# Performance work log

Measured on AMD Instinct MI355X. Metric: run time of the kernel, lower is better.

The kernel has to match this reference:

```python
import jax, jax.numpy as jnp
import numpy as np

B, S, D, H = 2, 2048, 1024, 16
HD = D // H  # head dim = 64


def setup_inputs() -> dict:
    key = jax.random.key(0)
    k1, k2, k3, k4 = jax.random.split(key, 4)
    x = jax.random.normal(k1, (B, S, D), dtype=jnp.float32)
    context = jax.random.normal(k2, (B, S, D), dtype=jnp.float32)
    Wq = jax.random.normal(k3, (D, D), dtype=jnp.float32) * 0.02   # to_query weight [out,in]
    Wkv = jax.random.normal(k4, (2 * D, D), dtype=jnp.float32) * 0.02  # to_key_value weight [out,in]
    return {"x": x, "context": context, "Wq": Wq, "Wkv": Wkv}


def reference(x, context, Wq, Wkv):
    b, i, _ = x.shape
    j = context.shape[1]
    # projections (torch Linear: y = x @ W.T)
    q = x @ Wq.T                      # [b, i, D]
    kv = context @ Wkv.T              # [b, j, 2D]
    k, v = kv[..., :D], kv[..., D:]
    # split heads: (h c) ordering -> reshape last dim to [H, HD]
    q = q.reshape(b, i, H, HD).transpose(0, 2, 1, 3)  # [b,h,i,c]
    k = k.reshape(b, j, H, HD).transpose(0, 2, 1, 3)  # [b,h,j,c]
    v = v.reshape(b, j, H, HD).transpose(0, 2, 1, 3)  # [b,h,j,c]
    q = q * (HD ** -0.5)
    scores = jnp.einsum('bhic,bhjc->bhij', q, k)      # [b,h,i,j]
    scores = scores - jax.lax.stop_gradient(scores.max(axis=-1, keepdims=True))
    attn = jax.nn.softmax(scores, axis=-1)
    out = jnp.einsum('bhij,bhjc->bhic', attn, v)      # [b,h,i,c]
    out = out.transpose(0, 2, 1, 3).reshape(b, i, H * HD)  # 'b h n d -> b n (h d)'
    return out
```

## Files before the change

### kernel.cpp

```cpp
#include <hip/hip_runtime.h>
#include <hip/hip_bf16.h>
#include <stdint.h>

typedef unsigned short u16;
typedef __attribute__((ext_vector_type(8))) __bf16 bf16x8;
typedef __attribute__((ext_vector_type(4))) float f32x4;
typedef __attribute__((ext_vector_type(16))) float f32x16;

#define AS1(p) ((const __attribute__((address_space(1))) void*)(p))
#define AS3(p) ((__attribute__((address_space(3))) void*)(p))

__device__ __forceinline__ u16 f2bf(float f) {
  union { float f; uint32_t u; } c; c.f = f;
  uint32_t u = c.u;
  u += 0x7fffu + ((u >> 16) & 1u);
  return (u16)(u >> 16);
}

__device__ __forceinline__ float exp2_fast(float x) {
  float r; asm("v_exp_f32 %0, %1" : "=v"(r) : "v"(x)); return r;
}

__global__ __launch_bounds__(256) void cast4_f32_bf16(
    const float4* __restrict__ s0, ushort4* __restrict__ d0, int n0,
    const float4* __restrict__ s1, ushort4* __restrict__ d1, int n1,
    const float4* __restrict__ s2, ushort4* __restrict__ d2, int n2,
    const float4* __restrict__ s3, ushort4* __restrict__ d3, int n3) {
  int bid = blockIdx.x;
  const float4* src; ushort4* dst; int n4, b0, nb;
  if (bid < 512)       { src = s0; dst = d0; n4 = n0; b0 = 0;    nb = 512; }
  else if (bid < 1024) { src = s1; dst = d1; n4 = n1; b0 = 512;  nb = 512; }
  else if (bid < 1152) { src = s2; dst = d2; n4 = n2; b0 = 1024; nb = 128; }
  else                 { src = s3; dst = d3; n4 = n3; b0 = 1152; nb = 256; }
  int stride = nb * 256;
  for (int i = (bid - b0) * 256 + threadIdx.x; i < n4; i += stride) {
    float4 v = src[i];
    ushort4 o;
    o.x = f2bf(v.x); o.y = f2bf(v.y); o.z = f2bf(v.z); o.w = f2bf(v.w);
    dst[i] = o;
  }
}

__global__ __launch_bounds__(256) void gemm_fused(const u16* __restrict__ xb,
                                                  const u16* __restrict__ wqb,
                                                  u16* __restrict__ qo,
                                                  const u16* __restrict__ cb,
                                                  const u16* __restrict__ wkb,
                                                  u16* __restrict__ kvo,
                                                  float scale_q) {
  __shared__ u16 As[3][128 * 32];
  __shared__ u16 Bs[3][128 * 32];
  const int K = 1024;
  int bid = (blockIdx.x & 7) * 96 + (blockIdx.x >> 3);
  const u16 *A, *B; u16* C; int N, bm, bn; float scale;
  if (bid < 256) { A = xb; B = wqb; C = qo;  N = 1024; bm = bid >> 3; bn = bid & 7;  scale = scale_q; }
  else { int b2 = bid - 256; A = cb; B = wkb; C = kvo; N = 2048; bm = b2 >> 4; bn = b2 & 15; scale = 1.0f; }

  int tid = threadIdx.x;
  int w = tid >> 6, l = tid & 63;
  int wr = w >> 1, wc = w & 1;
  int lr = l & 15, lg = l >> 4;

  const u16* Abase = A + (size_t)(bm * 128 + (l >> 2)) * K + (l & 3) * 8;
  const u16* Bbase = B + (size_t)(bn * 128 + (l >> 2)) * K + (l & 3) * 8;

  f32x4 acc[4][4];
#pragma unroll
  for (int i = 0; i < 4; ++i)
#pragma unroll
    for (int j = 0; j < 4; ++j) acc[i][j] = (f32x4){0.f, 0.f, 0.f, 0.f};

#define STAGE(buf, k0)                                                              \
  {                                                                                 \
    _Pragma("unroll")                                                               \
    for (int t2 = 0; t2 < 2; ++t2) {                                                \
      int seg = w * 2 + t2;                                                         \
      __builtin_amdgcn_global_load_lds(AS1(Abase + (size_t)seg * 16 * K + (k0)),    \
                                       AS3(&As[buf][seg * 512]), 16, 0, 0);         \
      __builtin_amdgcn_global_load_lds(AS1(Bbase + (size_t)seg * 16 * K + (k0)),    \
                                       AS3(&Bs[buf][seg * 512]), 16, 0, 0);         \
    }                                                                               \
  }

  STAGE(0, 0);
  STAGE(1, 32);
  int cur = 0;
  for (int t = 0; t < 32; ++t) {
    if (t < 30) {
      int pf = cur + 2; if (pf >= 3) pf -= 3;
      STAGE(pf, (t + 2) * 32);
      asm volatile("s_waitcnt vmcnt(8)" ::: "memory");
    } else if (t == 30) {
      asm volatile("s_waitcnt vmcnt(4)" ::: "memory");
    } else {
      asm volatile("s_waitcnt vmcnt(0)" ::: "memory");
    }
    __builtin_amdgcn_s_barrier();
    bf16x8 af[4], bb[4];
#pragma unroll
    for (int i = 0; i < 4; ++i)
      af[i] = *(const bf16x8*)(&As[cur][(wr * 64 + i * 16 + lr) * 32 + lg * 8]);
#pragma unroll
    for (int j = 0; j < 4; ++j)
      bb[j] = *(const bf16x8*)(&Bs[cur][(wc * 64 + j * 16 + lr) * 32 + lg * 8]);
    asm volatile("s_waitcnt lgkmcnt(0)" ::: "memory");
    __builtin_amdgcn_sched_barrier(0);
#pragma unroll
    for (int i = 0; i < 4; ++i)
#pragma unroll
      for (int j = 0; j < 4; ++j)
        acc[i][j] = __builtin_amdgcn_mfma_f32_16x16x32_bf16(af[i], bb[j], acc[i][j], 0, 0, 0);
    __builtin_amdgcn_s_barrier();
    if (++cur == 3) cur = 0;
  }
#undef STAGE

#pragma unroll
  for (int i = 0; i < 4; ++i)
#pragma unroll
    for (int j = 0; j < 4; ++j)
#pragma unroll
      for (int r = 0; r < 4; ++r) {
        int row = bm * 128 + wr * 64 + i * 16 + lg * 4 + r;
        int col = bn * 128 + wc * 64 + j * 16 + lr;
        C[(size_t)row * N + col] = f2bf(acc[i][j][r] * scale);
      }
}

#define SQ 2048
#define NTT 16

__global__ __launch_bounds__(256, 2) void attn_kernel(const u16* __restrict__ Q,
                                                      const u16* __restrict__ KV,
                                                      float* __restrict__ O) {
  __shared__ u16 Ks[2][128 * 64];
  __shared__ u16 Vt[64 * 128];

  int wgid = (blockIdx.x & 7) * 64 + (blockIdx.x >> 3);
  int qt = wgid & 15;
  int bh = wgid >> 4;
  int b = bh >> 4, h = bh & 15;
  int tid = threadIdx.x;
  int w = tid >> 6, l = tid & 63;
  int li = l & 31, hi = l >> 5;
  int jr = l >> 3, bk = l & 7;
  int a7 = tid & 7, jj = tid >> 3;

  const u16* kbase = KV + (size_t)b * SQ * 2048 + (size_t)h * 64;
  const u16* vbase = kbase + 1024;
  int i0g = qt * 128 + w * 32;
  const u16* qrow = Q + (size_t)(b * SQ + i0g + li) * 1024 + h * 64;

  bf16x8 qf0 = *(const bf16x8*)(qrow + 0  + hi * 8);
  bf16x8 qf1 = *(const bf16x8*)(qrow + 16 + hi * 8);
  bf16x8 qf2 = *(const bf16x8*)(qrow + 32 + hi * 8);
  bf16x8 qf3 = *(const bf16x8*)(qrow + 48 + hi * 8);

  union { u16 u[8]; bf16x8 v; } onesu;
#pragma unroll
  for (int e = 0; e < 8; ++e) onesu.u[e] = 0x3F80;
  bf16x8 ones = onesu.v;

#pragma unroll
  for (int c = 0; c < 4; ++c) {
    const u16* gk = kbase + (size_t)(c * 32 + w * 8 + jr) * 2048 + ((bk ^ jr) * 8);
    __builtin_amdgcn_global_load_lds(AS1(gk), AS3(&Ks[0][c * 2048 + w * 512]), 16, 0, 0);
  }
  uint4 vrA = *(const uint4*)(vbase + (size_t)(jj +  0) * 2048 + a7 * 8);
  uint4 vrB = *(const uint4*)(vbase + (size_t)(jj + 32) * 2048 + a7 * 8);
  uint4 vrC = *(const uint4*)(vbase + (size_t)(jj + 64) * 2048 + a7 * 8);
  uint4 vrD = *(const uint4*)(vbase + (size_t)(jj + 96) * 2048 + a7 * 8);

  float m_run = -1e30f;
  f32x16 acc0, acc1, accS, zz;
#pragma unroll
  for (int r = 0; r < 16; ++r) { acc0[r] = 0.f; acc1[r] = 0.f; accS[r] = 0.f; zz[r] = 0.f; }

  int swk = (li & 7) << 4;
  int sw0 = ((li ^ (li >> 3)) & 7) << 4;
  int sw1 = (((32 + li) ^ ((32 + li) >> 3)) & 7) << 4;

  for (int t = 0; t < NTT; ++t) {
    u16* Ksc = (u16*)Ks[t & 1];
    char* Vtc = (char*)Vt;
    __syncthreads();
    {
      const u16* pA = (const u16*)&vrA;
      const u16* pB = (const u16*)&vrB;
      const u16* pC = (const u16*)&vrC;
      const u16* pD = (const u16*)&vrD;
#pragma unroll
      for (int e = 0; e < 8; ++e) {
        int dbyte = (a7 * 8 + e) * 256, sw = (e ^ a7) << 4;
        *(u16*)(Vtc + dbyte + (((jj * 2) +   0) ^ sw)) = pA[e];
        *(u16*)(Vtc + dbyte + (((jj * 2) +  64) ^ sw)) = pB[e];
        *(u16*)(Vtc + dbyte + (((jj * 2) + 128) ^ sw)) = pC[e];
        *(u16*)(Vtc + dbyte + (((jj * 2) + 192) ^ sw)) = pD[e];
      }
    }
    asm volatile("s_waitcnt lgkmcnt(0)" ::: "memory");
    __builtin_amdgcn_s_barrier();
    if (t + 1 < NTT) {
      int j0n = (t + 1) * 128;
      u16* Ksn = (u16*)Ks[(t + 1) & 1];
#pragma unroll
      for (int c = 0; c < 4; ++c) {
        const u16* gk = kbase + (size_t)(j0n + c * 32 + w * 8 + jr) * 2048 + ((bk ^ jr) * 8);
        __builtin_amdgcn_global_load_lds(AS1(gk), AS3(&Ksn[c * 2048 + w * 512]), 16, 0, 0);
      }
      vrA = *(const uint4*)(vbase + (size_t)(j0n + jj +  0) * 2048 + a7 * 8);
      vrB = *(const uint4*)(vbase + (size_t)(j0n + jj + 32) * 2048 + a7 * 8);
      vrC = *(const uint4*)(vbase + (size_t)(j0n + jj + 64) * 2048 + a7 * 8);
      vrD = *(const uint4*)(vbase + (size_t)(j0n + jj + 96) * 2048 + a7 * 8);
    }
    f32x16 s0, s1, s2, s3;
    __builtin_amdgcn_s_setprio(1);
#define QKT1(sv, JB)                                                             \
    {                                                                            \
      const char* kr = (const char*)Ksc + ((JB) * 32 + li) * 128;                \
      bf16x8 kk;                                                                 \
      kk = *(const bf16x8*)(kr + ((0  + hi * 16) ^ swk));                        \
      sv = __builtin_amdgcn_mfma_f32_32x32x16_bf16(kk, qf0, zz, 0, 0, 0);        \
      kk = *(const bf16x8*)(kr + ((32 + hi * 16) ^ swk));                        \
      sv = __builtin_amdgcn_mfma_f32_32x32x16_bf16(kk, qf1, sv, 0, 0, 0);        \
      kk = *(const bf16x8*)(kr + ((64 + hi * 16) ^ swk));                        \
      sv = __builtin_amdgcn_mfma_f32_32x32x16_bf16(kk, qf2, sv, 0, 0, 0);        \
      kk = *(const bf16x8*)(kr + ((96 + hi * 16) ^ swk));                        \
      sv = __builtin_amdgcn_mfma_f32_32x32x16_bf16(kk, qf3, sv, 0, 0, 0);        \
    }
    QKT1(s0, 0)
    QKT1(s1, 1)
    QKT1(s2, 2)
    QKT1(s3, 3)
#undef QKT1
    __builtin_amdgcn_s_setprio(0);
    float pm = fmaxf(s0[14], s0[15]);
#pragma unroll
    for (int r = 0; r < 14; r += 2) pm = fmaxf(fmaxf(pm, s0[r]), s0[r + 1]);
#pragma unroll
    for (int r = 0; r < 16; r += 2) pm = fmaxf(fmaxf(pm, s1[r]), s1[r + 1]);
#pragma unroll
    for (int r = 0; r < 16; r += 2) pm = fmaxf(fmaxf(pm, s2[r]), s2[r + 1]);
#pragma unroll
    for (int r = 0; r < 16; r += 2) pm = fmaxf(fmaxf(pm, s3[r]), s3[r + 1]);
    pm = fmaxf(pm, __shfl_xor(pm, 32));
    if (!__all(pm <= m_run + 8.0f)) {
      float mnew = fmaxf(m_run, pm);
      float esc = exp2_fast(m_run - mnew);
      m_run = mnew;
      accS[0] *= esc;
#pragma unroll
      for (int r = 0; r < 16; ++r) { acc0[r] *= esc; acc1[r] *= esc; }
    }
#pragma unroll
    for (int r = 0; r < 16; ++r) s0[r] = exp2_fast(s0[r] - m_run);
#pragma unroll
    for (int r = 0; r < 16; ++r) s1[r] = exp2_fast(s1[r] - m_run);
#pragma unroll
    for (int r = 0; r < 16; ++r) s2[r] = exp2_fast(s2[r] - m_run);
#pragma unroll
    for (int r = 0; r < 16; ++r) s3[r] = exp2_fast(s3[r] - m_run);
    unsigned pw[32];
#pragma unroll
    for (int i2 = 0; i2 < 8; ++i2) {
      asm("v_cvt_pk_bf16_f32 %0, %1, %2" : "=v"(pw[i2])      : "v"(s0[2 * i2]), "v"(s0[2 * i2 + 1]));
      asm("v_cvt_pk_bf16_f32 %0, %1, %2" : "=v"(pw[8 + i2])  : "v"(s1[2 * i2]), "v"(s1[2 * i2 + 1]));
      asm("v_cvt_pk_bf16_f32 %0, %1, %2" : "=v"(pw[16 + i2]) : "v"(s2[2 * i2]), "v"(s2[2 * i2 + 1]));
      asm("v_cvt_pk_bf16_f32 %0, %1, %2" : "=v"(pw[24 + i2]) : "v"(s3[2 * i2]), "v"(s3[2 * i2 + 1]));
    }
#pragma unroll
    for (int gB = 0; gB < 4; ++gB) {
      int o = gB * 8;
      asm volatile("v_permlane32_swap_b32 %0, %1" : "+v"(pw[o + 0]), "+v"(pw[o + 2]));
      asm volatile("v_permlane32_swap_b32 %0, %1" : "+v"(pw[o + 1]), "+v"(pw[o + 3]));
      asm volatile("v_permlane32_swap_b32 %0, %1" : "+v"(pw[o + 4]), "+v"(pw[o + 6]));
      asm volatile("v_permlane32_swap_b32 %0, %1" : "+v"(pw[o + 5]), "+v"(pw[o + 7]));
    }
    __builtin_amdgcn_s_setprio(1);
#pragma unroll
    for (int jsp = 0; jsp < 8; ++jsp) {
      uint4 ufr;
      ufr.x = pw[jsp * 4 + 0]; ufr.y = pw[jsp * 4 + 1];
      ufr.z = pw[jsp * 4 + 2]; ufr.w = pw[jsp * 4 + 3];
      bf16x8 pa = *(bf16x8*)&ufr;
      int jbyte = jsp * 32 + hi * 16;
      bf16x8 v0 = *(const bf16x8*)(Vtc + li * 256 + (jbyte ^ sw0));
      bf16x8 v1 = *(const bf16x8*)(Vtc + (32 + li) * 256 + (jbyte ^ sw1));
      acc0 = __builtin_amdgcn_mfma_f32_32x32x16_bf16(v0, pa, acc0, 0, 0, 0);
      acc1 = __builtin_amdgcn_mfma_f32_32x32x16_bf16(v1, pa, acc1, 0, 0, 0);
      accS = __builtin_amdgcn_mfma_f32_32x32x16_bf16(ones, pa, accS, 0, 0, 0);
    }
    __builtin_amdgcn_s_setprio(0);
  }
  float inv = 1.f / accS[0];
  float* orow = O + ((size_t)(b * SQ + i0g + li) * 1024 + h * 64);
#pragma unroll
  for (int g = 0; g < 4; ++g) {
    f32x4 o0, o1;
#pragma unroll
    for (int q_ = 0; q_ < 4; ++q_) {
      o0[q_] = acc0[g * 4 + q_] * inv;
      o1[q_] = acc1[g * 4 + q_] * inv;
    }
    *(f32x4*)(orow + 8 * g + 4 * hi) = o0;
    *(f32x4*)(orow + 32 + 8 * g + 4 * hi) = o1;
  }
}

extern "C" void kernel_launch(void* const* d_in, const int* in_sizes, int n_in,
                              void* d_out, int out_size, void* d_ws, size_t ws_size,
                              hipStream_t stream) {
  (void)in_sizes; (void)n_in; (void)out_size; (void)ws_size;
  const float* x   = (const float*)d_in[0];
  const float* ctx = (const float*)d_in[1];
  const float* Wq  = (const float*)d_in[2];
  const float* Wkv = (const float*)d_in[3];
  float* out = (float*)d_out;
  char* ws = (char*)d_ws;

  u16* xb  = (u16*)(ws);
  u16* cb  = (u16*)(ws + (8ull  << 20));
  u16* wqb = (u16*)(ws + (16ull << 20));
  u16* wkb = (u16*)(ws + (18ull << 20));
  u16* q   = (u16*)(ws + (22ull << 20));
  u16* kv  = (u16*)(ws + (30ull << 20));

  cast4_f32_bf16<<<1408, 256, 0, stream>>>(
      (const float4*)x,   (ushort4*)xb,  (4096 * 1024) / 4,
      (const float4*)ctx, (ushort4*)cb,  (4096 * 1024) / 4,
      (const float4*)Wq,  (ushort4*)wqb, (1024 * 1024) / 4,
      (const float4*)Wkv, (ushort4*)wkb, (2048 * 1024) / 4);

  gemm_fused<<<768, 256, 0, stream>>>(xb, wqb, q, cb, wkb, kv, 0.125f * 1.44269504f);

  attn_kernel<<<512, 256, 0, stream>>>(q, kv, out);
}
```

Baseline: 99.72 us.

## Restructure projection GEMM to 256x256 tiles with 8 waves and swizzled LDS

The projection GEMM moves from 128x128 tiles with 4 waves and K-step 32 to 256x256 tiles with 8 waves, K-step 64 and double-buffered LDS. Global-to-LDS staging is split across four sub-phases interleaved with the MFMA groups, shared-memory chunks are XOR-swizzled to avoid bank conflicts, and setprio raises priority around the MFMA blocks. The aim is more data reuse per loaded byte and better overlap of memory and compute. The cost is only 192 workgroups on a GPU with many CUs, which leaves fewer waves to hide latency and adds many barriers per iteration.

```diff
diff --git a/kernel.cpp b/kernel.cpp
--- a/kernel.cpp
+++ b/kernel.cpp
@@ -41,88 +41,122 @@
   }
 }
 
-__global__ __launch_bounds__(256) void gemm_fused(const u16* __restrict__ xb,
-                                                  const u16* __restrict__ wqb,
-                                                  u16* __restrict__ qo,
-                                                  const u16* __restrict__ cb,
-                                                  const u16* __restrict__ wkb,
-                                                  u16* __restrict__ kvo,
-                                                  float scale_q) {
-  __shared__ u16 As[3][128 * 32];
-  __shared__ u16 Bs[3][128 * 32];
+__global__ __launch_bounds__(512, 2) void gemm_fused(const u16* __restrict__ xb,
+                                                     const u16* __restrict__ wqb,
+                                                     u16* __restrict__ qo,
+                                                     const u16* __restrict__ cb,
+                                                     const u16* __restrict__ wkb,
+                                                     u16* __restrict__ kvo,
+                                                     float scale_q) {
+  __shared__ u16 As[2][256 * 64];
+  __shared__ u16 Bs[2][256 * 64];
   const int K = 1024;
-  int bid = (blockIdx.x & 7) * 96 + (blockIdx.x >> 3);
+  int wg = (blockIdx.x & 7) * 24 + (blockIdx.x >> 3);
   const u16 *A, *B; u16* C; int N, bm, bn; float scale;
-  if (bid < 256) { A = xb; B = wqb; C = qo;  N = 1024; bm = bid >> 3; bn = bid & 7;  scale = scale_q; }
-  else { int b2 = bid - 256; A = cb; B = wkb; C = kvo; N = 2048; bm = b2 >> 4; bn = b2 & 15; scale = 1.0f; }
+  if (wg < 64) { A = xb; B = wqb; C = qo;  N = 1024; bm = wg >> 2; bn = wg & 3; scale = scale_q; }
+  else { int b2 = wg - 64; A = cb; B = wkb; C = kvo; N = 2048; bm = b2 >> 3; bn = b2 & 7; scale = 1.0f; }
 
   int tid = threadIdx.x;
-  int w = tid >> 6, l = tid & 63;
-  int wr = w >> 1, wc = w & 1;
+  int l = tid & 63;
+  int w = tid >> 6;
+  int wm = w >> 2, wn = w & 3;
   int lr = l & 15, lg = l >> 4;
 
-  const u16* Abase = A + (size_t)(bm * 128 + (l >> 2)) * K + (l & 3) * 8;
-  const u16* Bbase = B + (size_t)(bn * 128 + (l >> 2)) * K + (l & 3) * 8;
-
-  f32x4 acc[4][4];
-#pragma unroll
-  for (int i = 0; i < 4; ++i)
+  int srow = tid >> 3;
+  int schk = (tid & 7) ^ ((tid >> 3) & 7);
+  const u16* Asrc = A + (size_t)(bm * 256 + srow) * K + schk * 8;
+  const u16* Bsrc = B + (size_t)(bn * 256 + srow) * K + schk * 8;
+  int dsto = srow * 64 + (tid & 7) * 8;
+
+  auto stgA = [&](int buf, int kt, int r) {
+    __builtin_amdgcn_global_load_lds(AS1(Asrc + (size_t)r * 64 * K + kt * 64),
+                                     AS3(&As[buf][r * 64 * 64 + dsto]), 16, 0, 0);
+  };
+  auto stgB = [&](int buf, int kt, int r) {
+    __builtin_amdgcn_global_load_lds(AS1(Bsrc + (size_t)r * 64 * K + kt * 64),
+                                     AS3(&Bs[buf][r * 64 * 64 + dsto]), 16, 0, 0);
+  };
+
+  f32x4 acc[8][4];
+#pragma unroll
+  for (int i = 0; i < 8; ++i)
 #pragma unroll
     for (int j = 0; j < 4; ++j) acc[i][j] = (f32x4){0.f, 0.f, 0.f, 0.f};
 
-#define STAGE(buf, k0)                                                              \
-  {                                                                                 \
-    _Pragma("unroll")                                                               \
-    for (int t2 = 0; t2 < 2; ++t2) {                                                \
-      int seg = w * 2 + t2;                                                         \
-      __builtin_amdgcn_global_load_lds(AS1(Abase + (size_t)seg * 16 * K + (k0)),    \
-                                       AS3(&As[buf][seg * 512]), 16, 0, 0);         \
-      __builtin_amdgcn_global_load_lds(AS1(Bbase + (size_t)seg * 16 * K + (k0)),    \
-                                       AS3(&Bs[buf][seg * 512]), 16, 0, 0);         \
-    }                                                                               \
-  }
-
-  STAGE(0, 0);
-  STAGE(1, 32);
-  int cur = 0;
-  for (int t = 0; t < 32; ++t) {
-    if (t < 30) {
-      int pf = cur + 2; if (pf >= 3) pf -= 3;
-      STAGE(pf, (t + 2) * 32);
-      asm volatile("s_waitcnt vmcnt(8)" ::: "memory");
-    } else if (t == 30) {
-      asm volatile("s_waitcnt vmcnt(4)" ::: "memory");
-    } else {
-      asm volatile("s_waitcnt vmcnt(0)" ::: "memory");
-    }
+  stgA(0, 0, 0); stgA(0, 0, 1); stgA(0, 0, 2); stgA(0, 0, 3);
+  stgB(0, 0, 0); stgB(0, 0, 1); stgB(0, 0, 2); stgB(0, 0, 3);
+
+  for (int kt = 0; kt < 16; ++kt) {
+    int buf = kt & 1, nb = buf ^ 1;
+    bf16x8 bfr[2][4], afr[2][2];
+    if (kt < 15) { stgA(nb, kt + 1, 0); stgA(nb, kt + 1, 1); }
+    if (kt < 15) asm volatile("s_waitcnt vmcnt(2)" ::: "memory");
+    else         asm volatile("s_waitcnt vmcnt(0)" ::: "memory");
     __builtin_amdgcn_s_barrier();
-    bf16x8 af[4], bb[4];
-#pragma unroll
-    for (int i = 0; i < 4; ++i)
-      af[i] = *(const bf16x8*)(&As[cur][(wr * 64 + i * 16 + lr) * 32 + lg * 8]);
-#pragma unroll
-    for (int j = 0; j < 4; ++j)
-      bb[j] = *(const bf16x8*)(&Bs[cur][(wc * 64 + j * 16 + lr) * 32 + lg * 8]);
+#pragma unroll
+    for (int s = 0; s < 2; ++s)
+#pragma unroll
+      for (int j = 0; j < 4; ++j) {
+        int R = wn * 64 + j * 16 + lr;
+        bfr[s][j] = *(const bf16x8*)(&Bs[buf][R * 64 + ((s * 4 + lg) ^ (R & 7)) * 8]);
+      }
+#pragma unroll
+    for (int s = 0; s < 2; ++s)
+#pragma unroll
+      for (int ii = 0; ii < 2; ++ii) {
+        int R = wm * 128 + ii * 16 + lr;
+        afr[s][ii] = *(const bf16x8*)(&As[buf][R * 64 + ((s * 4 + lg) ^ (R & 7)) * 8]);
+      }
     asm volatile("s_waitcnt lgkmcnt(0)" ::: "memory");
     __builtin_amdgcn_sched_barrier(0);
-#pragma unroll
-    for (int i = 0; i < 4; ++i)
-#pragma unroll
-      for (int j = 0; j < 4; ++j)
-        acc[i][j] = __builtin_amdgcn_mfma_f32_16x16x32_bf16(af[i], bb[j], acc[i][j], 0, 0, 0);
+    __builtin_amdgcn_s_setprio(1);
+#pragma unroll
+    for (int ii = 0; ii < 2; ++ii)
+#pragma unroll
+      for (int j = 0; j < 4; ++j) {
+        acc[ii][j] = __builtin_amdgcn_mfma_f32_16x16x32_bf16(afr[0][ii], bfr[0][j], acc[ii][j], 0, 0, 0);
+        acc[ii][j] = __builtin_amdgcn_mfma_f32_16x16x32_bf16(afr[1][ii], bfr[1][j], acc[ii][j], 0, 0, 0);
+      }
+    __builtin_amdgcn_s_setprio(0);
     __builtin_amdgcn_s_barrier();
-    if (++cur == 3) cur = 0;
-  }
-#undef STAGE
-
-#pragma unroll
-  for (int i = 0; i < 4; ++i)
+#pragma unroll
+    for (int p = 1; p < 4; ++p) {
+#pragma unroll
+      for (int s = 0; s < 2; ++s)
+#pragma unroll
+        for (int ii = 0; ii < 2; ++ii) {
+          int R = wm * 128 + (2 * p + ii) * 16 + lr;
+          afr[s][ii] = *(const bf16x8*)(&As[buf][R * 64 + ((s * 4 + lg) ^ (R & 7)) * 8]);
+        }
+      if (kt < 15) {
+        if (p == 1)      { stgA(nb, kt + 1, 2); stgA(nb, kt + 1, 3); }
+        else if (p == 2) { stgB(nb, kt + 1, 0); stgB(nb, kt + 1, 1); }
+        else             { stgB(nb, kt + 1, 2); stgB(nb, kt + 1, 3); }
+      }
+      __builtin_amdgcn_s_barrier();
+      asm volatile("s_waitcnt lgkmcnt(0)" ::: "memory");
+      __builtin_amdgcn_sched_barrier(0);
+      __builtin_amdgcn_s_setprio(1);
+#pragma unroll
+      for (int ii = 0; ii < 2; ++ii)
+#pragma unroll
+        for (int j = 0; j < 4; ++j) {
+          acc[2 * p + ii][j] = __builtin_amdgcn_mfma_f32_16x16x32_bf16(afr[0][ii], bfr[0][j], acc[2 * p + ii][j], 0, 0, 0);
+          acc[2 * p + ii][j] = __builtin_amdgcn_mfma_f32_16x16x32_bf16(afr[1][ii], bfr[1][j], acc[2 * p + ii][j], 0, 0, 0);
+        }
+      __builtin_amdgcn_s_setprio(0);
+      __builtin_amdgcn_s_barrier();
+    }
+  }
+
+#pragma unroll
+  for (int i = 0; i < 8; ++i)
 #pragma unroll
     for (int j = 0; j < 4; ++j)
 #pragma unroll
       for (int r = 0; r < 4; ++r) {
-        int row = bm * 128 + wr * 64 + i * 16 + lg * 4 + r;
-        int col = bn * 128 + wc * 64 + j * 16 + lr;
+        int row = bm * 256 + wm * 128 + i * 16 + lg * 4 + r;
+        int col = bn * 256 + wn * 64 + j * 16 + lr;
         C[(size_t)row * N + col] = f2bf(acc[i][j][r] * scale);
       }
 }
@@ -331,7 +365,7 @@
       (const float4*)Wq,  (ushort4*)wqb, (1024 * 1024) / 4,
       (const float4*)Wkv, (ushort4*)wkb, (2048 * 1024) / 4);
 
-  gemm_fused<<<768, 256, 0, stream>>>(xb, wqb, q, cb, wkb, kv, 0.125f * 1.44269504f);
+  gemm_fused<<<192, 512, 0, stream>>>(xb, wqb, q, cb, wkb, kv, 0.125f * 1.44269504f);
 
   attn_kernel<<<512, 256, 0, stream>>>(q, kv, out);
 }
```

Result: slower. 102.6 us (+2.9%).
